# Kernel tuning notes

Measured on AMD Instinct MI355X. Metric: run time of the kernel, lower is better.

## Reference

```python
import jax, jax.numpy as jnp
import numpy as np

H = 51  # hidden size hardcoded in the module


def _lstm_cell(x, h, c, W_ih, b_ih, W_hh, b_hh):
    # PyTorch LSTMCell: gates in i, f, g, o order
    gates = x @ W_ih.T + b_ih + h @ W_hh.T + b_hh  # [B, 4H]
    i, f, g, o = jnp.split(gates, 4, axis=-1)
    i = jax.nn.sigmoid(i)
    f = jax.nn.sigmoid(f)
    g = jnp.tanh(g)
    o = jax.nn.sigmoid(o)
    c_new = f * c + i * g
    h_new = o * jnp.tanh(c_new)
    return h_new, c_new


def setup_inputs() -> dict:
    key = jax.random.key(0)
    ks = jax.random.split(key, 12)
    B, T = 2048, 256
    s1 = 1.0 / np.sqrt(H)
    u = lambda k, shape: jax.random.uniform(k, shape, jnp.float32, -s1, s1)
    return {
        "inputs": jax.random.normal(ks[0], (B, T), jnp.float32),
        "W_ih1": u(ks[1], (4 * H, 1)),
        "b_ih1": u(ks[2], (4 * H,)),
        "W_hh1": u(ks[3], (4 * H, H)),
        "b_hh1": u(ks[4], (4 * H,)),
        "W_ih2": u(ks[5], (4 * H, H)),
        "b_ih2": u(ks[6], (4 * H,)),
        "W_hh2": u(ks[7], (4 * H, H)),
        "b_hh2": u(ks[8], (4 * H,)),
        "W_lin": u(ks[9], (1, H)),
        "b_lin": u(ks[10], (1,)),
        "future": 16,
    }


def reference(inputs, W_ih1, b_ih1, W_hh1, b_hh1, W_ih2, b_ih2, W_hh2, b_hh2,
              W_lin, b_lin, future):
    B, T = inputs.shape
    h1 = jnp.zeros((B, H), inputs.dtype)
    c1 = jnp.zeros((B, H), inputs.dtype)
    h2 = jnp.zeros((B, H), inputs.dtype)
    c2 = jnp.zeros((B, H), inputs.dtype)

    def core(x_t, h1, c1, h2, c2):
        h1, c1 = _lstm_cell(x_t, h1, c1, W_ih1, b_ih1, W_hh1, b_hh1)
        h2, c2 = _lstm_cell(h1, h2, c2, W_ih2, b_ih2, W_hh2, b_hh2)
        out = h2 @ W_lin.T + b_lin  # [B, 1]
        return out, h1, c1, h2, c2

    def step(carry, x_t):
        h1, c1, h2, c2, _ = carry
        out, h1, c1, h2, c2 = core(x_t, h1, c1, h2, c2)
        return (h1, c1, h2, c2, out), out

    xs = inputs.T[:, :, None]  # [T, B, 1]
    init_out = jnp.zeros((B, 1), inputs.dtype)
    carry, outs_seen = jax.lax.scan(step, (h1, c1, h2, c2, init_out), xs)

    def fstep(carry, _):
        h1, c1, h2, c2, out = carry
        out, h1, c1, h2, c2 = core(out, h1, c1, h2, c2)
        return (h1, c1, h2, c2, out), out

    if future > 0:
        _, outs_fut = jax.lax.scan(fstep, carry, None, length=future)
        outs = jnp.concatenate([outs_seen, outs_fut], axis=0)  # [T+F, B, 1]
    else:
        outs = outs_seen
    return outs[:, :, 0].T  # [B, T+future]
```

## Files before the change

### kernel.cpp

```cpp
#include <hip/hip_runtime.h>
#include <math.h>

#define H 51
#define TSEEN 256
#define FUT 16
#define TTOT (TSEEN + FUT)
#define NB 8
#define THREADS 512
#define NWAVE 8
#define UPW 7
#define NBLOCKS (2048 / NB)

typedef _Float16 f16;
typedef _Float16 f16x8 __attribute__((ext_vector_type(8)));
typedef float f32x4 __attribute__((ext_vector_type(4)));

__device__ __forceinline__ float fast_rcp(float x) { return __builtin_amdgcn_rcpf(x); }
__device__ __forceinline__ float sigf(float x) {
  return fast_rcp(1.f + __expf(-x));
}
__device__ __forceinline__ float tanhf_(float x) {
  return fmaf(2.f, fast_rcp(1.f + __expf(-2.f * x)), -1.f);
}

__device__ __forceinline__ float xor8f(float v) {
  return __int_as_float(__builtin_amdgcn_mov_dpp(__float_as_int(v), 0x128, 0xf, 0xf, true));
}

#define MFMA __builtin_amdgcn_mfma_f32_16x16x32_f16

__launch_bounds__(THREADS, 2)
__global__ void lstm2_kernel(const float* __restrict__ inp,
                             const float* __restrict__ Wih1,
                             const float* __restrict__ bih1,
                             const float* __restrict__ Whh1,
                             const float* __restrict__ bhh1,
                             const float* __restrict__ Wih2,
                             const float* __restrict__ bih2,
                             const float* __restrict__ Whh2,
                             const float* __restrict__ bhh2,
                             const float* __restrict__ Wlin,
                             const float* __restrict__ blin,
                             float* __restrict__ out)
{
  __shared__ __align__(16) f16 Bh1[2][2][2][64][8];
  __shared__ __align__(16) f16 Bh2[2][2][2][64][8];
  __shared__ __align__(16) float xs[TSEEN][NB];
  __shared__ float parts[2][NWAVE][NB];
  __shared__ float outb[TTOT][NB];

  const int tid  = threadIdx.x;
  const int wv   = tid >> 6;
  const int lane = tid & 63;
  const int l15  = lane & 15;
  const int g4   = lane >> 4;
  const int bq   = l15 & 7;
  const bool mhi = (l15 & 8) != 0;
  const int baseb = blockIdx.x * NB;

  {
    f16* b1 = &Bh1[0][0][0][0][0];
    f16* b2 = &Bh2[0][0][0][0][0];
    for (int i = tid; i < 2 * 2 * 2 * 64 * 8; i += THREADS) {
      b1[i] = (f16)0.f; b2[i] = (f16)0.f;
    }
  }
  for (int i = tid; i < NB * TSEEN; i += THREADS) {
    int b = i >> 8, t = i & 255;
    xs[t][b] = inp[(size_t)(baseb + b) * TSEEN + t];
  }
  if (tid < 2 * NWAVE * NB) (&parts[0][0][0])[tid] = 0.f;

  f16x8 A1[2][2], A2[2][2], A3[2][2];
  #pragma unroll
  for (int m = 0; m < 2; ++m) {
    const int slotA = 4 * m + (l15 >> 2);
    const int uA = UPW * wv + slotA;
    const int gA = l15 & 3;
    const bool vA = (slotA < UPW) && (uA < H);
    const int row = gA * H + (vA ? uA : 0);
    #pragma unroll
    for (int kt = 0; kt < 2; ++kt) {
      #pragma unroll
      for (int j = 0; j < 8; ++j) {
        const int k = 32 * kt + 8 * g4 + j;
        float w1 = 0.f, w2 = 0.f, w3 = 0.f;
        if (vA) {
          if (k < H) {
            w1 = Whh1[row * H + k];
            w2 = Wih2[row * H + k];
            w3 = Whh2[row * H + k];
          } else if (k == H) {
            w1 = Wih1[row];
          }
        }
        A1[m][kt][j] = (f16)w1;
        A2[m][kt][j] = (f16)w2;
        A3[m][kt][j] = (f16)w3;
      }
    }
  }

  f32x4 bias1[2], bias2[2];
  #pragma unroll
  for (int m = 0; m < 2; ++m) {
    const int ulC = 4 * m + g4;
    const int u = UPW * wv + ulC;
    const bool v = (ulC < UPW) && (u < H);
    #pragma unroll
    for (int r = 0; r < 4; ++r) {
      const int rr = r * H + (v ? u : 0);
      bias1[m][r] = v ? (bih1[rr] + bhh1[rr]) : 0.f;
      bias2[m][r] = v ? (bih2[rr] + bhh2[rr]) : 0.f;
    }
  }

  const int slotC = (mhi ? 4 : 0) + g4;
  const int uC0 = UPW * wv + slotC;
  const bool vC = (slotC < UPW) && (uC0 < H);
  const int uC = vC ? uC0 : 0;
  const float wl = vC ? Wlin[uC] : 0.f;
  const float bl = blin[0];
  const int wkt = uC >> 5;
  const int wln = bq + 16 * ((uC >> 3) & 3);
  const int wj  = uC & 7;

  float c1 = 0.f, c2 = 0.f;
  const f32x4 zf = {0.f, 0.f, 0.f, 0.f};

  __syncthreads();
  if (tid < NB) {
    float x0 = xs[0][tid];
    f16 xh = (f16)x0;
    Bh1[1][0][1][tid + 32][3] = xh;
    Bh1[1][1][1][tid + 32][3] = (f16)(x0 - (float)xh);
  }
  __syncthreads();

  #pragma unroll 1
  for (int t = 0; t < TTOT; ++t) {
    const int pw = t & 1, pr = pw ^ 1;

    const f16x8 b1h0 = *(const f16x8*)&Bh1[pr][0][0][lane][0];
    const f16x8 b1h1 = *(const f16x8*)&Bh1[pr][0][1][lane][0];
    const f16x8 b1l0 = *(const f16x8*)&Bh1[pr][1][0][lane][0];
    const f16x8 b1l1 = *(const f16x8*)&Bh1[pr][1][1][lane][0];

    f32x4 ac1[2];
    #pragma unroll
    for (int m = 0; m < 2; ++m) {
      f32x4 hiC = MFMA(A1[m][0], b1h0, bias1[m], 0, 0, 0);
      hiC = MFMA(A1[m][1], b1h1, hiC, 0, 0, 0);
      f32x4 loC = MFMA(A1[m][0], b1l0, zf, 0, 0, 0);
      loC = MFMA(A1[m][1], b1l1, loC, 0, 0, 0);
      ac1[m] = hiC + loC;
    }

    float q0, q1, q2, q3;
    {
      float e0 = xor8f(ac1[1][0]);
      float e1 = xor8f(ac1[1][1]);
      float e2 = xor8f(ac1[1][2]);
      float e3 = xor8f(ac1[1][3]);
      q0 = mhi ? e0 : ac1[0][0];
      q1 = mhi ? e1 : ac1[0][1];
      q2 = mhi ? e2 : ac1[0][2];
      q3 = mhi ? e3 : ac1[0][3];
    }
    {
      float iv = sigf(q0), fv = sigf(q1);
      float gv = tanhf_(q2), ov = sigf(q3);
      c1 = fmaf(fv, c1, iv * gv);
      float h1n = ov * tanhf_(c1);
      if (vC) {
        f16 hh = (f16)h1n;
        Bh1[pw][0][wkt][wln][wj] = hh;
        Bh1[pw][1][wkt][wln][wj] = (f16)(h1n - (float)hh);
      }
    }
    if (t + 1 < TSEEN && tid < NB) {
      float xn = xs[t + 1][tid];
      f16 xh = (f16)xn;
      Bh1[pw][0][1][tid + 32][3] = xh;
      Bh1[pw][1][1][tid + 32][3] = (f16)(xn - (float)xh);
    }
    __syncthreads();

    if (t >= 1 && t < TSEEN && tid < NB) {
      float s = bl;
      #pragma unroll
      for (int w = 0; w < NWAVE; ++w) s += parts[pr][w][tid];
      outb[t - 1][tid] = s;
    }

    const f16x8 b2h0 = *(const f16x8*)&Bh2[pr][0][0][lane][0];
    const f16x8 b2h1 = *(const f16x8*)&Bh2[pr][0][1][lane][0];
    const f16x8 b2l0 = *(const f16x8*)&Bh2[pr][1][0][lane][0];
    const f16x8 b2l1 = *(const f16x8*)&Bh2[pr][1][1][lane][0];
    const f16x8 f1h0 = *(const f16x8*)&Bh1[pw][0][0][lane][0];
    const f16x8 f1h1 = *(const f16x8*)&Bh1[pw][0][1][lane][0];
    const f16x8 f1l0 = *(const f16x8*)&Bh1[pw][1][0][lane][0];
    const f16x8 f1l1 = *(const f16x8*)&Bh1[pw][1][1][lane][0];

    f32x4 ac2[2];
    #pragma unroll
    for (int m = 0; m < 2; ++m) {
      f32x4 rA = MFMA(A3[m][0], b2h0, bias2[m], 0, 0, 0);
      rA = MFMA(A3[m][1], b2h1, rA, 0, 0, 0);
      f32x4 rB = MFMA(A3[m][0], b2l0, zf, 0, 0, 0);
      rB = MFMA(A3[m][1], b2l1, rB, 0, 0, 0);
      f32x4 rC = MFMA(A2[m][0], f1h0, zf, 0, 0, 0);
      rC = MFMA(A2[m][1], f1h1, rC, 0, 0, 0);
      f32x4 rD = MFMA(A2[m][0], f1l0, zf, 0, 0, 0);
      rD = MFMA(A2[m][1], f1l1, rD, 0, 0, 0);
      ac2[m] = (rA + rB) + (rC + rD);
    }

    {
      float e0 = xor8f(ac2[1][0]);
      float e1 = xor8f(ac2[1][1]);
      float e2 = xor8f(ac2[1][2]);
      float e3 = xor8f(ac2[1][3]);
      q0 = mhi ? e0 : ac2[0][0];
      q1 = mhi ? e1 : ac2[0][1];
      q2 = mhi ? e2 : ac2[0][2];
      q3 = mhi ? e3 : ac2[0][3];
    }
    float pv;
    {
      float iv = sigf(q0), fv = sigf(q1);
      float gv = tanhf_(q2), ov = sigf(q3);
      c2 = fmaf(fv, c2, iv * gv);
      float h2n = ov * tanhf_(c2);
      pv = wl * h2n;
      if (vC) {
        f16 hh = (f16)h2n;
        Bh2[pw][0][wkt][wln][wj] = hh;
        Bh2[pw][1][wkt][wln][wj] = (f16)(h2n - (float)hh);
      }
    }
    pv += xor8f(pv);
    pv += __shfl_xor(pv, 16, 64);
    pv += __shfl_xor(pv, 32, 64);
    if (lane < NB) parts[pw][wv][lane] = pv;

    if (t >= TSEEN - 1) {
      __syncthreads();
      if (tid < NB) {
        float fbv = bl;
        #pragma unroll
        for (int w = 0; w < NWAVE; ++w) fbv += parts[pw][w][tid];
        outb[t][tid] = fbv;
        if (t < TTOT - 1) {
          f16 xh = (f16)fbv;
          Bh1[pw][0][1][tid + 32][3] = xh;
          Bh1[pw][1][1][tid + 32][3] = (f16)(fbv - (float)xh);
        }
      }
      __syncthreads();
    }
  }

  __syncthreads();
  for (int i = tid; i < TTOT * NB; i += THREADS) {
    int b = i / TTOT, t = i - b * TTOT;
    out[(size_t)(baseb + b) * TTOT + t] = outb[t][b];
  }
}

extern "C" void kernel_launch(void* const* d_in, const int* in_sizes, int n_in,
                              void* d_out, int out_size, void* d_ws, size_t ws_size,
                              hipStream_t stream) {
  (void)in_sizes; (void)n_in; (void)d_ws; (void)ws_size; (void)out_size;
  const float* inp  = (const float*)d_in[0];
  const float* Wih1 = (const float*)d_in[1];
  const float* bih1 = (const float*)d_in[2];
  const float* Whh1 = (const float*)d_in[3];
  const float* bhh1 = (const float*)d_in[4];
  const float* Wih2 = (const float*)d_in[5];
  const float* bih2 = (const float*)d_in[6];
  const float* Whh2 = (const float*)d_in[7];
  const float* bhh2 = (const float*)d_in[8];
  const float* Wlin = (const float*)d_in[9];
  const float* blin = (const float*)d_in[10];
  float* outp = (float*)d_out;

  lstm2_kernel<<<NBLOCKS, THREADS, 0, stream>>>(
      inp, Wih1, bih1, Whh1, bhh1, Wih2, bih2, Whh2, bhh2, Wlin, blin, outp);
}
```

Before: 288.6 us.

## Pack hi/lo fp16 split into spare MFMA batch columns to halve MFMA count

With NB=8, half of the 16 N-columns of each 16x16x32 MFMA were idle, so the fp16 hi and lo residual parts of h and x now go into columns 0-7 and 8-15 of a single B tile instead of separate buffers. This halves the MFMA count per step and the LDS reads for B operands, and the two halves are recombined with an xor-8 lane shuffle add. Bias is added only in the low half to avoid double counting. The cost is extra cross-lane shuffles and adds per gate before the activations.

```diff
diff --git a/kernel.cpp b/kernel.cpp
--- a/kernel.cpp
+++ b/kernel.cpp
@@ -43,8 +43,8 @@
                              const float* __restrict__ blin,
                              float* __restrict__ out)
 {
-  __shared__ __align__(16) f16 Bh1[2][2][2][64][8];
-  __shared__ __align__(16) f16 Bh2[2][2][2][64][8];
+  __shared__ __align__(16) f16 Bh1[2][2][64][8];
+  __shared__ __align__(16) f16 Bh2[2][2][64][8];
   __shared__ __align__(16) float xs[TSEEN][NB];
   __shared__ float parts[2][NWAVE][NB];
   __shared__ float outb[TTOT][NB];
@@ -59,9 +59,9 @@
   const int baseb = blockIdx.x * NB;
 
   {
-    f16* b1 = &Bh1[0][0][0][0][0];
-    f16* b2 = &Bh2[0][0][0][0][0];
-    for (int i = tid; i < 2 * 2 * 2 * 64 * 8; i += THREADS) {
+    f16* b1 = &Bh1[0][0][0][0];
+    f16* b2 = &Bh2[0][0][0][0];
+    for (int i = tid; i < 2 * 2 * 64 * 8; i += THREADS) {
       b1[i] = (f16)0.f; b2[i] = (f16)0.f;
     }
   }
@@ -106,7 +106,7 @@
   for (int m = 0; m < 2; ++m) {
     const int ulC = 4 * m + g4;
     const int u = UPW * wv + ulC;
-    const bool v = (ulC < UPW) && (u < H);
+    const bool v = (ulC < UPW) && (u < H) && (l15 < 8);
     #pragma unroll
     for (int r = 0; r < 4; ++r) {
       const int rr = r * H + (v ? u : 0);
@@ -126,14 +126,13 @@
   const int wj  = uC & 7;
 
   float c1 = 0.f, c2 = 0.f;
-  const f32x4 zf = {0.f, 0.f, 0.f, 0.f};
 
   __syncthreads();
   if (tid < NB) {
     float x0 = xs[0][tid];
     f16 xh = (f16)x0;
-    Bh1[1][0][1][tid + 32][3] = xh;
-    Bh1[1][1][1][tid + 32][3] = (f16)(x0 - (float)xh);
+    Bh1[1][1][tid + 32][3] = xh;
+    Bh1[1][1][tid + 40][3] = (f16)(x0 - (float)xh);
   }
   __syncthreads();
 
@@ -141,31 +140,30 @@
   for (int t = 0; t < TTOT; ++t) {
     const int pw = t & 1, pr = pw ^ 1;
 
-    const f16x8 b1h0 = *(const f16x8*)&Bh1[pr][0][0][lane][0];
-    const f16x8 b1h1 = *(const f16x8*)&Bh1[pr][0][1][lane][0];
-    const f16x8 b1l0 = *(const f16x8*)&Bh1[pr][1][0][lane][0];
-    const f16x8 b1l1 = *(const f16x8*)&Bh1[pr][1][1][lane][0];
+    const f16x8 b1k0 = *(const f16x8*)&Bh1[pr][0][lane][0];
+    const f16x8 b1k1 = *(const f16x8*)&Bh1[pr][1][lane][0];
 
     f32x4 ac1[2];
     #pragma unroll
     for (int m = 0; m < 2; ++m) {
-      f32x4 hiC = MFMA(A1[m][0], b1h0, bias1[m], 0, 0, 0);
-      hiC = MFMA(A1[m][1], b1h1, hiC, 0, 0, 0);
-      f32x4 loC = MFMA(A1[m][0], b1l0, zf, 0, 0, 0);
-      loC = MFMA(A1[m][1], b1l1, loC, 0, 0, 0);
-      ac1[m] = hiC + loC;
+      f32x4 c = MFMA(A1[m][0], b1k0, bias1[m], 0, 0, 0);
+      ac1[m] = MFMA(A1[m][1], b1k1, c, 0, 0, 0);
     }
 
     float q0, q1, q2, q3;
     {
-      float e0 = xor8f(ac1[1][0]);
-      float e1 = xor8f(ac1[1][1]);
-      float e2 = xor8f(ac1[1][2]);
-      float e3 = xor8f(ac1[1][3]);
-      q0 = mhi ? e0 : ac1[0][0];
-      q1 = mhi ? e1 : ac1[0][1];
-      q2 = mhi ? e2 : ac1[0][2];
-      q3 = mhi ? e3 : ac1[0][3];
+      float s00 = ac1[0][0] + xor8f(ac1[0][0]);
+      float s01 = ac1[0][1] + xor8f(ac1[0][1]);
+      float s02 = ac1[0][2] + xor8f(ac1[0][2]);
+      float s03 = ac1[0][3] + xor8f(ac1[0][3]);
+      float s10 = ac1[1][0] + xor8f(ac1[1][0]);
+      float s11 = ac1[1][1] + xor8f(ac1[1][1]);
+      float s12 = ac1[1][2] + xor8f(ac1[1][2]);
+      float s13 = ac1[1][3] + xor8f(ac1[1][3]);
+      q0 = mhi ? s10 : s00;
+      q1 = mhi ? s11 : s01;
+      q2 = mhi ? s12 : s02;
+      q3 = mhi ? s13 : s03;
     }
     {
       float iv = sigf(q0), fv = sigf(q1);
@@ -174,15 +172,15 @@
       float h1n = ov * tanhf_(c1);
       if (vC) {
         f16 hh = (f16)h1n;
-        Bh1[pw][0][wkt][wln][wj] = hh;
-        Bh1[pw][1][wkt][wln][wj] = (f16)(h1n - (float)hh);
+        Bh1[pw][wkt][wln][wj]     = hh;
+        Bh1[pw][wkt][wln + 8][wj] = (f16)(h1n - (float)hh);
       }
     }
     if (t + 1 < TSEEN && tid < NB) {
       float xn = xs[t + 1][tid];
       f16 xh = (f16)xn;
-      Bh1[pw][0][1][tid + 32][3] = xh;
-      Bh1[pw][1][1][tid + 32][3] = (f16)(xn - (float)xh);
+      Bh1[pw][1][tid + 32][3] = xh;
+      Bh1[pw][1][tid + 40][3] = (f16)(xn - (float)xh);
     }
     __syncthreads();
 
@@ -193,38 +191,33 @@
       outb[t - 1][tid] = s;
     }
 
-    const f16x8 b2h0 = *(const f16x8*)&Bh2[pr][0][0][lane][0];
-    const f16x8 b2h1 = *(const f16x8*)&Bh2[pr][0][1][lane][0];
-    const f16x8 b2l0 = *(const f16x8*)&Bh2[pr][1][0][lane][0];
-    const f16x8 b2l1 = *(const f16x8*)&Bh2[pr][1][1][lane][0];
-    const f16x8 f1h0 = *(const f16x8*)&Bh1[pw][0][0][lane][0];
-    const f16x8 f1h1 = *(const f16x8*)&Bh1[pw][0][1][lane][0];
-    const f16x8 f1l0 = *(const f16x8*)&Bh1[pw][1][0][lane][0];
-    const f16x8 f1l1 = *(const f16x8*)&Bh1[pw][1][1][lane][0];
+    const f16x8 b2k0 = *(const f16x8*)&Bh2[pr][0][lane][0];
+    const f16x8 b2k1 = *(const f16x8*)&Bh2[pr][1][lane][0];
+    const f16x8 f1k0 = *(const f16x8*)&Bh1[pw][0][lane][0];
+    const f16x8 f1k1 = *(const f16x8*)&Bh1[pw][1][lane][0];
 
     f32x4 ac2[2];
     #pragma unroll
     for (int m = 0; m < 2; ++m) {
-      f32x4 rA = MFMA(A3[m][0], b2h0, bias2[m], 0, 0, 0);
-      rA = MFMA(A3[m][1], b2h1, rA, 0, 0, 0);
-      f32x4 rB = MFMA(A3[m][0], b2l0, zf, 0, 0, 0);
-      rB = MFMA(A3[m][1], b2l1, rB, 0, 0, 0);
-      f32x4 rC = MFMA(A2[m][0], f1h0, zf, 0, 0, 0);
-      rC = MFMA(A2[m][1], f1h1, rC, 0, 0, 0);
-      f32x4 rD = MFMA(A2[m][0], f1l0, zf, 0, 0, 0);
-      rD = MFMA(A2[m][1], f1l1, rD, 0, 0, 0);
-      ac2[m] = (rA + rB) + (rC + rD);
-    }
-
-    {
-      float e0 = xor8f(ac2[1][0]);
-      float e1 = xor8f(ac2[1][1]);
-      float e2 = xor8f(ac2[1][2]);
-      float e3 = xor8f(ac2[1][3]);
-      q0 = mhi ? e0 : ac2[0][0];
-      q1 = mhi ? e1 : ac2[0][1];
-      q2 = mhi ? e2 : ac2[0][2];
-      q3 = mhi ? e3 : ac2[0][3];
+      f32x4 c = MFMA(A3[m][0], b2k0, bias2[m], 0, 0, 0);
+      c = MFMA(A3[m][1], b2k1, c, 0, 0, 0);
+      c = MFMA(A2[m][0], f1k0, c, 0, 0, 0);
+      ac2[m] = MFMA(A2[m][1], f1k1, c, 0, 0, 0);
+    }
+
+    {
+      float s00 = ac2[0][0] + xor8f(ac2[0][0]);
+      float s01 = ac2[0][1] + xor8f(ac2[0][1]);
+      float s02 = ac2[0][2] + xor8f(ac2[0][2]);
+      float s03 = ac2[0][3] + xor8f(ac2[0][3]);
+      float s10 = ac2[1][0] + xor8f(ac2[1][0]);
+      float s11 = ac2[1][1] + xor8f(ac2[1][1]);
+      float s12 = ac2[1][2] + xor8f(ac2[1][2]);
+      float s13 = ac2[1][3] + xor8f(ac2[1][3]);
+      q0 = mhi ? s10 : s00;
+      q1 = mhi ? s11 : s01;
+      q2 = mhi ? s12 : s02;
+      q3 = mhi ? s13 : s03;
     }
     float pv;
     {
@@ -235,8 +228,8 @@
       pv = wl * h2n;
       if (vC) {
         f16 hh = (f16)h2n;
-        Bh2[pw][0][wkt][wln][wj] = hh;
-        Bh2[pw][1][wkt][wln][wj] = (f16)(h2n - (float)hh);
+        Bh2[pw][wkt][wln][wj]     = hh;
+        Bh2[pw][wkt][wln + 8][wj] = (f16)(h2n - (float)hh);
       }
     }
     pv += xor8f(pv);
@@ -253,8 +246,8 @@
         outb[t][tid] = fbv;
         if (t < TTOT - 1) {
           f16 xh = (f16)fbv;
-          Bh1[pw][0][1][tid + 32][3] = xh;
-          Bh1[pw][1][1][tid + 32][3] = (f16)(fbv - (float)xh);
+          Bh1[pw][1][tid + 32][3] = xh;
+          Bh1[pw][1][tid + 40][3] = (f16)(fbv - (float)xh);
         }
       }
       __syncthreads();
```

New measurement: 232.6 us. -19.4%, faster.
